# Optimization experiments

Measured on AMD Instinct MI355X. Metric: run time of the kernel, lower is better.

## Reference

```python
import jax, jax.numpy as jnp
import numpy as np

B, S, D, H = 4, 2048, 1024, 16
DK = D // H


def setup_inputs() -> dict:
    key = jax.random.key(0)
    ks = jax.random.split(key, 8)
    q = jax.random.normal(ks[0], (B, S, D), dtype=jnp.float32)
    k = jax.random.normal(ks[1], (B, S, D), dtype=jnp.float32)
    v = jax.random.normal(ks[2], (B, S, D), dtype=jnp.float32)
    mask = jnp.ones((1, 1, S, S), dtype=jnp.int32)
    scale = 1.0 / np.sqrt(D)
    Wq = jax.random.normal(ks[3], (D, D), dtype=jnp.float32) * scale
    Wk = jax.random.normal(ks[4], (D, D), dtype=jnp.float32) * scale
    Wv = jax.random.normal(ks[5], (D, D), dtype=jnp.float32) * scale
    Wo = jax.random.normal(ks[6], (D, D), dtype=jnp.float32) * scale
    return {"q": q, "k": k, "v": v, "mask": mask,
            "Wq": Wq, "Wk": Wk, "Wv": Wv, "Wo": Wo}


def reference(q, k, v, mask, Wq, Wk, Wv, Wo):
    # Linear projections (nn.Linear with bias=False: x @ W.T)
    query = jnp.einsum('bsd,ed->bse', q, Wq).reshape(B, S, H, DK).transpose(0, 2, 1, 3)
    key_ = jnp.einsum('bsd,ed->bse', k, Wk).reshape(B, S, H, DK).transpose(0, 2, 1, 3)
    value = jnp.einsum('bsd,ed->bse', v, Wv).reshape(B, S, H, DK).transpose(0, 2, 1, 3)
    # scores: [B, H, S, S]
    scores = jnp.einsum('bhqd,bhkd->bhqk', query, key_) / jnp.sqrt(jnp.float32(DK))
    scores = jnp.where(mask == 0, jnp.float32(-1e9), scores)
    attn = jax.nn.softmax(scores, axis=-1)
    # context: [B, H, S, DK] -> [B, S, D]
    ctx = jnp.einsum('bhqk,bhkd->bhqd', attn, value)
    ctx = ctx.transpose(0, 2, 1, 3).reshape(B, S, D)
    return jnp.einsum('bsd,ed->bse', ctx, Wo)
```

## Files before the change

### kernel.cpp

```cpp
#include <hip/hip_runtime.h>
#include <hip/hip_bf16.h>
#include <stdint.h>

#define Bb 4
#define Ss 2048
#define Dd 1024
#define Hh 16
#define DK 64

typedef short bf16x8 __attribute__((ext_vector_type(8)));
typedef float f32x4 __attribute__((ext_vector_type(4)));
typedef float f32x16 __attribute__((ext_vector_type(16)));
typedef unsigned short u16;
typedef unsigned int u32;

__device__ __forceinline__ u16 f2bf(float f) {
  u32 u = __float_as_uint(f);
  u32 r = (u + 0x7fffu + ((u >> 16) & 1u)) >> 16;
  return (u16)r;
}

#define CVTPK(d_, lo_, hi_) asm("v_cvt_pk_bf16_f32 %0, %1, %2" : "=v"(d_) : "v"(lo_), "v"(hi_))

#define GLD16(g, l) __builtin_amdgcn_global_load_lds( \
    (const __attribute__((address_space(1))) u32*)(g), \
    (__attribute__((address_space(3))) u32*)(l), 16, 0, 0)

__global__ __launch_bounds__(256) void cvt4_kernel(const float* __restrict__ a, const float* __restrict__ b,
                                                   const float* __restrict__ c, const float* __restrict__ d,
                                                   u16* __restrict__ oa, u16* __restrict__ ob,
                                                   u16* __restrict__ oc, u16* __restrict__ od) {
  int which = blockIdx.y;
  const float* in = which == 0 ? a : which == 1 ? b : which == 2 ? c : d;
  u16* out = which == 0 ? oa : which == 1 ? ob : which == 2 ? oc : od;
  int i = (blockIdx.x * 256 + threadIdx.x) * 4;
  float4 v = *(const float4*)(in + i);
  ushort4 o;
  o.x = f2bf(v.x); o.y = f2bf(v.y); o.z = f2bf(v.z); o.w = f2bf(v.w);
  *(ushort4*)(out + i) = o;
}

__device__ __forceinline__ void regstage_f32(char* dst, const float* __restrict__ src,
                                             int base, int K, int k0, int tid) {
#pragma unroll
  for (int rr = 0; rr < 8; ++rr) {
    int off = rr * 4096 + tid * 16;
    int row = off >> 8;
    int c4 = off & 255;
    f32x4 vv = *(const f32x4*)(src + (size_t)(base + row) * K + k0 + (c4 >> 2));
    u32 lo_, hi_;
    CVTPK(lo_, vv[0], vv[1]);
    CVTPK(hi_, vv[2], vv[3]);
    uint2 val; val.x = lo_; val.y = hi_;
    *(uint2*)(dst + row * 128 + ((c4 >> 1) ^ ((row & 7) << 4))) = val;
  }
}

template <int F32A, int F32W, int OUT_BF16, int TAU, int HEAVY_M>
__device__ __forceinline__ void gemm_body(char* smem, int ord,
                                          const void* __restrict__ Ain,
                                          const void* __restrict__ Win,
                                          void* __restrict__ Cout,
                                          int M, int N, int K, float scale) {
  char* As = smem;
  char* Wl = smem + 16384;
  const int tid = threadIdx.x;
  const int lane = tid & 63;
  const int wv = tid >> 6;
  const int wm = wv >> 1, wn = wv & 1;
  const int heavy = ((ord & 7) << 3) | (ord >> 6);
  const int light = (ord >> 3) & 7;
  const int m0 = (HEAVY_M ? heavy : light) * 128;
  const int n0 = (HEAVY_M ? light : heavy) * 128;

  f32x4 acc[4][4] = {};

  for (int k0 = 0; k0 < K; k0 += 64) {
    if constexpr (F32A) {
      regstage_f32(As, (const float*)Ain, m0, K, k0, tid);
    } else {
      const u16* Ab = (const u16*)Ain;
#pragma unroll
      for (int c = 0; c < 4; ++c) {
        int tb = c * 4096 + tid * 16;
        int row = tb >> 7;
        int sg = (tb & 127) ^ ((row & 7) << 4);
        GLD16(Ab + (size_t)(m0 + row) * K + k0 + (sg >> 1), As + c * 4096 + wv * 1024);
      }
    }
    if constexpr (F32W) {
      regstage_f32(Wl, (const float*)Win, n0, K, k0, tid);
    } else {
      const u16* Wb = (const u16*)Win;
#pragma unroll
      for (int c = 0; c < 4; ++c) {
        int tb = c * 4096 + tid * 16;
        int row = tb >> 7;
        int sg = (tb & 127) ^ ((row & 7) << 4);
        GLD16(Wb + (size_t)(n0 + row) * K + k0 + (sg >> 1), Wl + c * 4096 + wv * 1024);
      }
    }
    __syncthreads();
#pragma unroll
    for (int kk = 0; kk < 2; ++kk) {
      bf16x8 af[4], bfr[4];
#pragma unroll
      for (int mi = 0; mi < 4; ++mi) {
        int r = wm * 64 + mi * 16 + (lane & 15);
        int cb = kk * 64 + (lane >> 4) * 16;
        af[mi] = *(const bf16x8*)(As + r * 128 + (cb ^ ((r & 7) << 4)));
      }
#pragma unroll
      for (int ni = 0; ni < 4; ++ni) {
        int r = wn * 64 + ni * 16 + (lane & 15);
        int cb = kk * 64 + (lane >> 4) * 16;
        bfr[ni] = *(const bf16x8*)(Wl + r * 128 + (cb ^ ((r & 7) << 4)));
      }
#pragma unroll
      for (int mi = 0; mi < 4; ++mi)
#pragma unroll
        for (int ni = 0; ni < 4; ++ni)
          acc[mi][ni] = __builtin_amdgcn_mfma_f32_16x16x32_bf16(af[mi], bfr[ni], acc[mi][ni], 0, 0, 0);
    }
    __syncthreads();
  }
  int l4 = lane & 15;
  int cst = TAU ? ((l4 & 3) | ((l4 & 4) << 1) | ((l4 & 8) >> 1)) : l4;
#pragma unroll
  for (int mi = 0; mi < 4; ++mi) {
#pragma unroll
    for (int i = 0; i < 4; ++i) {
      int row = m0 + wm * 64 + mi * 16 + (lane >> 4) * 4 + i;
#pragma unroll
      for (int ni = 0; ni < 4; ++ni) {
        int col = n0 + wn * 64 + ni * 16 + cst;
        float val = acc[mi][ni][i] * scale;
        if (OUT_BF16)
          ((u16*)Cout)[(size_t)row * N + col] = f2bf(val);
        else
          ((float*)Cout)[(size_t)row * N + col] = val;
      }
    }
  }
}

__global__ __launch_bounds__(256) void proj_fused(const float* __restrict__ q,
                                                  const float* __restrict__ k,
                                                  const float* __restrict__ v,
                                                  const u16* __restrict__ Wqb,
                                                  const u16* __restrict__ Wkb,
                                                  const u16* __restrict__ Wvb,
                                                  u16* __restrict__ Qp,
                                                  u16* __restrict__ Kp,
                                                  u16* __restrict__ VT,
                                                  float qscale) {
  __shared__ __align__(16) char smem[32768];
  const int ord = blockIdx.x;
  const int which = ord >> 9;
  const int local = ord & 511;
  if (which == 0)
    gemm_body<1, 0, 1, 0, 1>(smem, local, q, Wqb, Qp, 8192, 1024, 1024, qscale);
  else if (which == 1)
    gemm_body<1, 0, 1, 0, 1>(smem, local, k, Wkb, Kp, 8192, 1024, 1024, 1.0f);
  else
    gemm_body<0, 1, 1, 1, 0>(smem, local, Wvb, v, VT, 1024, 8192, 1024, 1.0f);
}

__global__ __launch_bounds__(256) void gemm_out(const u16* __restrict__ A,
                                                const u16* __restrict__ W,
                                                float* __restrict__ Cout) {
  __shared__ __align__(16) char smem[32768];
  gemm_body<0, 0, 0, 0, 1>(smem, blockIdx.x, A, W, Cout, 8192, 1024, 1024, 1.0f);
}

#define MAKE_PA(dst, P, R0)                                       \
  {                                                               \
    u32 W0_, W1_, W2_, W3_;                                       \
    CVTPK(W0_, P[R0 + 0], P[R0 + 1]);                             \
    CVTPK(W1_, P[R0 + 2], P[R0 + 3]);                             \
    CVTPK(W2_, P[R0 + 4], P[R0 + 5]);                             \
    CVTPK(W3_, P[R0 + 6], P[R0 + 7]);                             \
    union { u32 w[4]; bf16x8 v; } u_;                             \
    u_.w[0] = W0_; u_.w[1] = W1_; u_.w[2] = W2_; u_.w[3] = W3_;   \
    dst = u_.v;                                                   \
  }

__global__ __launch_bounds__(512) void attn_kernel(const u16* __restrict__ Q,
                                                   const u16* __restrict__ Kp,
                                                   const u16* __restrict__ VT,
                                                   u16* __restrict__ ctx) {
  __shared__ __align__(16) char lds[32768];
  const int tid = threadIdx.x;
  const int lane = tid & 63;
  const int w = tid >> 6;
  const int hi = lane >> 5;
  const int lq = lane & 31;
  const int fid = blockIdx.x;
  const int bh = ((fid >> 6) << 3) | (fid & 7);
  const int qb = (fid >> 3) & 7;
  const int b = bh >> 4;
  const int h = bh & 15;
  const int q0 = qb * 256 + w * 32;

  const u16* qptr = Q + ((size_t)(b * Ss + q0 + lq)) * Dd + h * DK + hi * 8;
  bf16x8 qf[4];
#pragma unroll
  for (int ds = 0; ds < 4; ++ds) qf[ds] = *(const bf16x8*)(qptr + ds * 16);

  const int t16 = tid * 16;
  const int srow = t16 >> 7;
  const int colB = t16 & 127;
  const int scolB = colB ^ ((srow & 7) << 4);
  const u16* ksrc = Kp + ((size_t)(b * Ss + srow)) * Dd + h * DK + (scolB >> 1);
  const u16* vsrc = VT + ((size_t)(h * DK + srow)) * (Bb * Ss) + b * Ss + (scolB >> 1);

  f32x16 o0 = {}, o1 = {};
  float lsum = 0.f;
  const int xk = (lq & 7) << 4;

  GLD16(ksrc, lds + w * 1024);
  GLD16(vsrc, lds + 8192 + w * 1024);
  __syncthreads();

  for (int t = 0; t < Ss / 64; ++t) {
    const int buf = (t & 1) * 16384;
    if (t + 1 < Ss / 64) {
      const int nbuf = 16384 - buf;
      const size_t s0n = (size_t)(t + 1) * 64;
      GLD16(ksrc + s0n * Dd, lds + nbuf + w * 1024);
      GLD16(vsrc + s0n, lds + nbuf + 8192 + w * 1024);
    }
    f32x16 p0 = {}, p1 = {};
    __builtin_amdgcn_s_setprio(1);
#pragma unroll
    for (int ds = 0; ds < 4; ++ds) {
      const int c = (32 * ds + 16 * hi) ^ xk;
      bf16x8 ka = *(const bf16x8*)(lds + buf + lq * 128 + c);
      bf16x8 kb = *(const bf16x8*)(lds + buf + 4096 + lq * 128 + c);
      p0 = __builtin_amdgcn_mfma_f32_32x32x16_bf16(ka, qf[ds], p0, 0, 0, 0);
      p1 = __builtin_amdgcn_mfma_f32_32x32x16_bf16(kb, qf[ds], p1, 0, 0, 0);
    }
    __builtin_amdgcn_s_setprio(0);
    bf16x8 va0 = *(const bf16x8*)(lds + buf + 8192 + lq * 128 + ((16 * hi) ^ xk));
    bf16x8 vb0 = *(const bf16x8*)(lds + buf + 8192 + 4096 + lq * 128 + ((16 * hi) ^ xk));
    float s16[16];
#pragma unroll
    for (int r = 0; r < 16; ++r) {
      p0[r] = __builtin_amdgcn_exp2f(p0[r]);
      p1[r] = __builtin_amdgcn_exp2f(p1[r]);
      s16[r] = p0[r] + p1[r];
    }
#pragma unroll
    for (int r = 0; r < 8; ++r) s16[r] += s16[r + 8];
#pragma unroll
    for (int r = 0; r < 4; ++r) s16[r] += s16[r + 4];
    lsum += (s16[0] + s16[2]) + (s16[1] + s16[3]);
    bf16x8 pa[4];
    MAKE_PA(pa[0], p0, 0);
    MAKE_PA(pa[1], p0, 8);
    MAKE_PA(pa[2], p1, 0);
    MAKE_PA(pa[3], p1, 8);
    __builtin_amdgcn_sched_barrier(0);
    asm volatile("s_nop 3");
    __builtin_amdgcn_s_setprio(1);
    o0 = __builtin_amdgcn_mfma_f32_32x32x16_bf16(va0, pa[0], o0, 0, 0, 0);
    o1 = __builtin_amdgcn_mfma_f32_32x32x16_bf16(vb0, pa[0], o1, 0, 0, 0);
#pragma unroll
    for (int ks = 1; ks < 4; ++ks) {
      const int c = (32 * ks + 16 * hi) ^ xk;
      bf16x8 va = *(const bf16x8*)(lds + buf + 8192 + lq * 128 + c);
      bf16x8 vb = *(const bf16x8*)(lds + buf + 8192 + 4096 + lq * 128 + c);
      o0 = __builtin_amdgcn_mfma_f32_32x32x16_bf16(va, pa[ks], o0, 0, 0, 0);
      o1 = __builtin_amdgcn_mfma_f32_32x32x16_bf16(vb, pa[ks], o1, 0, 0, 0);
    }
    __builtin_amdgcn_s_setprio(0);
    __syncthreads();
  }

  lsum += __shfl_xor(lsum, 32);
  float inv = 1.f / lsum;
  u16* cptr = ctx + ((size_t)(b * Ss + q0 + lq)) * Dd + h * DK + 4 * hi;
#pragma unroll
  for (int g = 0; g < 4; ++g) {
    ushort4 s0v, s1v;
    s0v.x = f2bf(o0[4 * g + 0] * inv);
    s0v.y = f2bf(o0[4 * g + 1] * inv);
    s0v.z = f2bf(o0[4 * g + 2] * inv);
    s0v.w = f2bf(o0[4 * g + 3] * inv);
    *(ushort4*)(cptr + 8 * g) = s0v;
    s1v.x = f2bf(o1[4 * g + 0] * inv);
    s1v.y = f2bf(o1[4 * g + 1] * inv);
    s1v.z = f2bf(o1[4 * g + 2] * inv);
    s1v.w = f2bf(o1[4 * g + 3] * inv);
    *(ushort4*)(cptr + 32 + 8 * g) = s1v;
  }
}

extern "C" void kernel_launch(void* const* d_in, const int* in_sizes, int n_in,
                              void* d_out, int out_size, void* d_ws, size_t ws_size,
                              hipStream_t stream) {
  const float* q = (const float*)d_in[0];
  const float* k = (const float*)d_in[1];
  const float* v = (const float*)d_in[2];
  const float* Wq = (const float*)d_in[4];
  const float* Wk = (const float*)d_in[5];
  const float* Wv = (const float*)d_in[6];
  const float* Wo = (const float*)d_in[7];

  u16* wsp = (u16*)d_ws;
  const size_t DDsz = (size_t)Dd * Dd;
  const size_t BSD = (size_t)Bb * Ss * Dd;
  u16* Wqb = wsp;
  u16* Wkb = wsp + DDsz;
  u16* Wvb = wsp + 2 * DDsz;
  u16* Wob = wsp + 3 * DDsz;
  u16* Qp = wsp + 4 * DDsz;
  u16* Kp = Qp + BSD;
  u16* VT = Kp + BSD;
  u16* Xb = VT + BSD;

  dim3 blk(256);
  cvt4_kernel<<<dim3(DDsz / 1024, 4), blk, 0, stream>>>(Wq, Wk, Wv, Wo, Wqb, Wkb, Wvb, Wob);

  const float QSCALE = 0.125f * 1.4426950408889634f;
  proj_fused<<<dim3(1536), blk, 0, stream>>>(q, k, v, Wqb, Wkb, Wvb, Qp, Kp, VT, QSCALE);

  attn_kernel<<<dim3(512), dim3(512), 0, stream>>>(Qp, Kp, VT, Xb);

  gemm_out<<<dim3(512), blk, 0, stream>>>(Xb, Wob, (float*)d_out);
}
```

Before: 197.5 us.

## Split attention KV loop across two wave halves and merge partial outputs in LDS

The attention block grows to 1024 threads. Each half of the waves handles half of the key/value sequence for the same 256 queries, using its own double-buffered LDS region. Partial outputs and row sums are combined through LDS at the end. This halves the serial KV loop length per wave and raises wave-level parallelism, at the cost of doubled LDS, extra syncs, and duplicated Q loads. There is no running max, so exp values are summed directly, which is valid because the softmax has no max subtraction.

```diff
diff --git a/kernel.cpp b/kernel.cpp
--- a/kernel.cpp
+++ b/kernel.cpp
@@ -185,14 +185,16 @@
     dst = u_.v;                                                   \
   }
 
-__global__ __launch_bounds__(512) void attn_kernel(const u16* __restrict__ Q,
-                                                   const u16* __restrict__ Kp,
-                                                   const u16* __restrict__ VT,
-                                                   u16* __restrict__ ctx) {
-  __shared__ __align__(16) char lds[32768];
+__global__ __launch_bounds__(1024, 8) void attn_kernel(const u16* __restrict__ Q,
+                                                       const u16* __restrict__ Kp,
+                                                       const u16* __restrict__ VT,
+                                                       u16* __restrict__ ctx) {
+  __shared__ __align__(64) char lds[65536];
   const int tid = threadIdx.x;
   const int lane = tid & 63;
   const int w = tid >> 6;
+  const int half = w >> 3;
+  const int qw = w & 7;
   const int hi = lane >> 5;
   const int lq = lane & 31;
   const int fid = blockIdx.x;
@@ -200,36 +202,40 @@
   const int qb = (fid >> 3) & 7;
   const int b = bh >> 4;
   const int h = bh & 15;
-  const int q0 = qb * 256 + w * 32;
+  const int q0 = qb * 256 + qw * 32;
 
   const u16* qptr = Q + ((size_t)(b * Ss + q0 + lq)) * Dd + h * DK + hi * 8;
   bf16x8 qf[4];
 #pragma unroll
   for (int ds = 0; ds < 4; ++ds) qf[ds] = *(const bf16x8*)(qptr + ds * 16);
 
-  const int t16 = tid * 16;
+  const int tl = tid & 511;
+  const int t16 = tl * 16;
   const int srow = t16 >> 7;
   const int colB = t16 & 127;
   const int scolB = colB ^ ((srow & 7) << 4);
   const u16* ksrc = Kp + ((size_t)(b * Ss + srow)) * Dd + h * DK + (scolB >> 1);
   const u16* vsrc = VT + ((size_t)(h * DK + srow)) * (Bb * Ss) + b * Ss + (scolB >> 1);
+  const int hbase = half * 32768;
+  const int wb = (tl >> 6) * 1024;
 
   f32x16 o0 = {}, o1 = {};
   float lsum = 0.f;
   const int xk = (lq & 7) << 4;
-
-  GLD16(ksrc, lds + w * 1024);
-  GLD16(vsrc, lds + 8192 + w * 1024);
+  const int tb0 = half * 16;
+
+#define STAGE_T(T, s) {                                                   \
+    size_t roff = (size_t)(T) * 64;                                       \
+    GLD16(ksrc + roff * Dd, lds + hbase + (s) * 16384 + wb);              \
+    GLD16(vsrc + roff, lds + hbase + (s) * 16384 + 8192 + wb);            \
+  }
+
+  STAGE_T(tb0, 0)
   __syncthreads();
 
-  for (int t = 0; t < Ss / 64; ++t) {
-    const int buf = (t & 1) * 16384;
-    if (t + 1 < Ss / 64) {
-      const int nbuf = 16384 - buf;
-      const size_t s0n = (size_t)(t + 1) * 64;
-      GLD16(ksrc + s0n * Dd, lds + nbuf + w * 1024);
-      GLD16(vsrc + s0n, lds + nbuf + 8192 + w * 1024);
-    }
+  for (int i = 0; i < 16; ++i) {
+    const int buf = hbase + (i & 1) * 16384;
+    if (i < 15) STAGE_T(tb0 + i + 1, (i + 1) & 1)
     f32x16 p0 = {}, p1 = {};
     __builtin_amdgcn_s_setprio(1);
 #pragma unroll
@@ -278,22 +284,43 @@
   }
 
   lsum += __shfl_xor(lsum, 32);
-  float inv = 1.f / lsum;
-  u16* cptr = ctx + ((size_t)(b * Ss + q0 + lq)) * Dd + h * DK + 4 * hi;
-#pragma unroll
-  for (int g = 0; g < 4; ++g) {
-    ushort4 s0v, s1v;
-    s0v.x = f2bf(o0[4 * g + 0] * inv);
-    s0v.y = f2bf(o0[4 * g + 1] * inv);
-    s0v.z = f2bf(o0[4 * g + 2] * inv);
-    s0v.w = f2bf(o0[4 * g + 3] * inv);
-    *(ushort4*)(cptr + 8 * g) = s0v;
-    s1v.x = f2bf(o1[4 * g + 0] * inv);
-    s1v.y = f2bf(o1[4 * g + 1] * inv);
-    s1v.z = f2bf(o1[4 * g + 2] * inv);
-    s1v.w = f2bf(o1[4 * g + 3] * inv);
-    *(ushort4*)(cptr + 32 + 8 * g) = s1v;
-  }
+
+  f32x16* ex = (f32x16*)lds;
+  float* exl = (float*)(lds + 32768);
+  if (half) {
+    ex[(w - 8) * 64 + lane] = o0;
+    exl[(w - 8) * 64 + lane] = lsum;
+  }
+  __syncthreads();
+  f32x16 oB0 = {};
+  float lB = 0.f;
+  if (!half) {
+    oB0 = ex[w * 64 + lane];
+    lB = exl[w * 64 + lane];
+  }
+  __syncthreads();
+  if (half) ex[(w - 8) * 64 + lane] = o1;
+  __syncthreads();
+  if (!half) {
+    f32x16 oB1 = ex[w * 64 + lane];
+    float inv = 1.f / (lsum + lB);
+    u16* cptr = ctx + ((size_t)(b * Ss + q0 + lq)) * Dd + h * DK + 4 * hi;
+#pragma unroll
+    for (int g = 0; g < 4; ++g) {
+      ushort4 s0v, s1v;
+      s0v.x = f2bf((o0[4 * g + 0] + oB0[4 * g + 0]) * inv);
+      s0v.y = f2bf((o0[4 * g + 1] + oB0[4 * g + 1]) * inv);
+      s0v.z = f2bf((o0[4 * g + 2] + oB0[4 * g + 2]) * inv);
+      s0v.w = f2bf((o0[4 * g + 3] + oB0[4 * g + 3]) * inv);
+      *(ushort4*)(cptr + 8 * g) = s0v;
+      s1v.x = f2bf((o1[4 * g + 0] + oB1[4 * g + 0]) * inv);
+      s1v.y = f2bf((o1[4 * g + 1] + oB1[4 * g + 1]) * inv);
+      s1v.z = f2bf((o1[4 * g + 2] + oB1[4 * g + 2]) * inv);
+      s1v.w = f2bf((o1[4 * g + 3] + oB1[4 * g + 3]) * inv);
+      *(ushort4*)(cptr + 32 + 8 * g) = s1v;
+    }
+  }
+#undef STAGE_T
 }
 
 extern "C" void kernel_launch(void* const* d_in, const int* in_sizes, int n_in,
@@ -325,7 +352,7 @@
   const float QSCALE = 0.125f * 1.4426950408889634f;
   proj_fused<<<dim3(1536), blk, 0, stream>>>(q, k, v, Wqb, Wkb, Wvb, Qp, Kp, VT, QSCALE);
 
-  attn_kernel<<<dim3(512), dim3(512), 0, stream>>>(Qp, Kp, VT, Xb);
+  attn_kernel<<<dim3(512), dim3(1024), 0, stream>>>(Qp, Kp, VT, Xb);
 
   gemm_out<<<dim3(512), blk, 0, stream>>>(Xb, Wob, (float*)d_out);
 }
```

Result: slower. 563.2 us (+185.1%).

## Process two KV tiles per barrier with four-slot LDS ring in attention

Applied to the files above, without the earlier changes.

The attention loop now stages two 64-row K/V tiles per iteration into a four-slot LDS ring (64KB) and computes both tiles between barriers. This halves the number of __syncthreads per head and issues prefetches two tiles ahead, aiming to hide global load latency and barrier stalls. The cost is doubled LDS use per block, which may reduce occupancy, and more code from the unrolled macro bodies.

```diff
diff --git a/kernel.cpp b/kernel.cpp
--- a/kernel.cpp
+++ b/kernel.cpp
@@ -185,11 +185,13 @@
     dst = u_.v;                                                   \
   }
 
+#define SLOT(U) (((((U) >> 1) & 1) << 15) | (((U) & 1) << 14))
+
 __global__ __launch_bounds__(512) void attn_kernel(const u16* __restrict__ Q,
                                                    const u16* __restrict__ Kp,
                                                    const u16* __restrict__ VT,
                                                    u16* __restrict__ ctx) {
-  __shared__ __align__(16) char lds[32768];
+  __shared__ __align__(16) char lds[65536];
   const int tid = threadIdx.x;
   const int lane = tid & 63;
   const int w = tid >> 6;
@@ -217,63 +219,73 @@
   f32x16 o0 = {}, o1 = {};
   float lsum = 0.f;
   const int xk = (lq & 7) << 4;
-
-  GLD16(ksrc, lds + w * 1024);
-  GLD16(vsrc, lds + 8192 + w * 1024);
+  const int wb = w * 1024;
+
+#define STAGE_U(U) {                                               \
+    size_t ro = (size_t)(U) * 64;                                  \
+    GLD16(ksrc + ro * Dd, lds + SLOT(U) + wb);                     \
+    GLD16(vsrc + ro, lds + SLOT(U) + 8192 + wb);                   \
+  }
+
+#define ATTN_TILE(BASE) {                                                             \
+    const int buf_ = (BASE);                                                          \
+    f32x16 p0 = {}, p1 = {};                                                          \
+    __builtin_amdgcn_s_setprio(1);                                                    \
+    _Pragma("unroll")                                                                 \
+    for (int ds = 0; ds < 4; ++ds) {                                                  \
+      const int c = (32 * ds + 16 * hi) ^ xk;                                         \
+      bf16x8 ka = *(const bf16x8*)(lds + buf_ + lq * 128 + c);                        \
+      bf16x8 kb = *(const bf16x8*)(lds + buf_ + 4096 + lq * 128 + c);                 \
+      p0 = __builtin_amdgcn_mfma_f32_32x32x16_bf16(ka, qf[ds], p0, 0, 0, 0);          \
+      p1 = __builtin_amdgcn_mfma_f32_32x32x16_bf16(kb, qf[ds], p1, 0, 0, 0);          \
+    }                                                                                 \
+    __builtin_amdgcn_s_setprio(0);                                                    \
+    bf16x8 va0 = *(const bf16x8*)(lds + buf_ + 8192 + lq * 128 + ((16 * hi) ^ xk));   \
+    bf16x8 vb0 = *(const bf16x8*)(lds + buf_ + 8192 + 4096 + lq * 128 + ((16 * hi) ^ xk)); \
+    float s16[16];                                                                    \
+    _Pragma("unroll")                                                                 \
+    for (int r = 0; r < 16; ++r) {                                                    \
+      p0[r] = __builtin_amdgcn_exp2f(p0[r]);                                          \
+      p1[r] = __builtin_amdgcn_exp2f(p1[r]);                                          \
+      s16[r] = p0[r] + p1[r];                                                         \
+    }                                                                                 \
+    _Pragma("unroll")                                                                 \
+    for (int r = 0; r < 8; ++r) s16[r] += s16[r + 8];                                 \
+    _Pragma("unroll")                                                                 \
+    for (int r = 0; r < 4; ++r) s16[r] += s16[r + 4];                                 \
+    lsum += (s16[0] + s16[2]) + (s16[1] + s16[3]);                                    \
+    bf16x8 pa[4];                                                                     \
+    MAKE_PA(pa[0], p0, 0);                                                            \
+    MAKE_PA(pa[1], p0, 8);                                                            \
+    MAKE_PA(pa[2], p1, 0);                                                            \
+    MAKE_PA(pa[3], p1, 8);                                                            \
+    __builtin_amdgcn_sched_barrier(0);                                                \
+    asm volatile("s_nop 3");                                                          \
+    __builtin_amdgcn_s_setprio(1);                                                    \
+    o0 = __builtin_amdgcn_mfma_f32_32x32x16_bf16(va0, pa[0], o0, 0, 0, 0);            \
+    o1 = __builtin_amdgcn_mfma_f32_32x32x16_bf16(vb0, pa[0], o1, 0, 0, 0);            \
+    _Pragma("unroll")                                                                 \
+    for (int ks = 1; ks < 4; ++ks) {                                                  \
+      const int c = (32 * ks + 16 * hi) ^ xk;                                         \
+      bf16x8 va = *(const bf16x8*)(lds + buf_ + 8192 + lq * 128 + c);                 \
+      bf16x8 vb = *(const bf16x8*)(lds + buf_ + 8192 + 4096 + lq * 128 + c);          \
+      o0 = __builtin_amdgcn_mfma_f32_32x32x16_bf16(va, pa[ks], o0, 0, 0, 0);          \
+      o1 = __builtin_amdgcn_mfma_f32_32x32x16_bf16(vb, pa[ks], o1, 0, 0, 0);          \
+    }                                                                                 \
+    __builtin_amdgcn_s_setprio(0);                                                    \
+  }
+
+  STAGE_U(0)
+  STAGE_U(1)
   __syncthreads();
 
-  for (int t = 0; t < Ss / 64; ++t) {
-    const int buf = (t & 1) * 16384;
-    if (t + 1 < Ss / 64) {
-      const int nbuf = 16384 - buf;
-      const size_t s0n = (size_t)(t + 1) * 64;
-      GLD16(ksrc + s0n * Dd, lds + nbuf + w * 1024);
-      GLD16(vsrc + s0n, lds + nbuf + 8192 + w * 1024);
-    }
-    f32x16 p0 = {}, p1 = {};
-    __builtin_amdgcn_s_setprio(1);
-#pragma unroll
-    for (int ds = 0; ds < 4; ++ds) {
-      const int c = (32 * ds + 16 * hi) ^ xk;
-      bf16x8 ka = *(const bf16x8*)(lds + buf + lq * 128 + c);
-      bf16x8 kb = *(const bf16x8*)(lds + buf + 4096 + lq * 128 + c);
-      p0 = __builtin_amdgcn_mfma_f32_32x32x16_bf16(ka, qf[ds], p0, 0, 0, 0);
-      p1 = __builtin_amdgcn_mfma_f32_32x32x16_bf16(kb, qf[ds], p1, 0, 0, 0);
-    }
-    __builtin_amdgcn_s_setprio(0);
-    bf16x8 va0 = *(const bf16x8*)(lds + buf + 8192 + lq * 128 + ((16 * hi) ^ xk));
-    bf16x8 vb0 = *(const bf16x8*)(lds + buf + 8192 + 4096 + lq * 128 + ((16 * hi) ^ xk));
-    float s16[16];
-#pragma unroll
-    for (int r = 0; r < 16; ++r) {
-      p0[r] = __builtin_amdgcn_exp2f(p0[r]);
-      p1[r] = __builtin_amdgcn_exp2f(p1[r]);
-      s16[r] = p0[r] + p1[r];
-    }
-#pragma unroll
-    for (int r = 0; r < 8; ++r) s16[r] += s16[r + 8];
-#pragma unroll
-    for (int r = 0; r < 4; ++r) s16[r] += s16[r + 4];
-    lsum += (s16[0] + s16[2]) + (s16[1] + s16[3]);
-    bf16x8 pa[4];
-    MAKE_PA(pa[0], p0, 0);
-    MAKE_PA(pa[1], p0, 8);
-    MAKE_PA(pa[2], p1, 0);
-    MAKE_PA(pa[3], p1, 8);
-    __builtin_amdgcn_sched_barrier(0);
-    asm volatile("s_nop 3");
-    __builtin_amdgcn_s_setprio(1);
-    o0 = __builtin_amdgcn_mfma_f32_32x32x16_bf16(va0, pa[0], o0, 0, 0, 0);
-    o1 = __builtin_amdgcn_mfma_f32_32x32x16_bf16(vb0, pa[0], o1, 0, 0, 0);
-#pragma unroll
-    for (int ks = 1; ks < 4; ++ks) {
-      const int c = (32 * ks + 16 * hi) ^ xk;
-      bf16x8 va = *(const bf16x8*)(lds + buf + 8192 + lq * 128 + c);
-      bf16x8 vb = *(const bf16x8*)(lds + buf + 8192 + 4096 + lq * 128 + c);
-      o0 = __builtin_amdgcn_mfma_f32_32x32x16_bf16(va, pa[ks], o0, 0, 0, 0);
-      o1 = __builtin_amdgcn_mfma_f32_32x32x16_bf16(vb, pa[ks], o1, 0, 0, 0);
-    }
-    __builtin_amdgcn_s_setprio(0);
+  for (int t = 0; t < 16; ++t) {
+    if (t < 15) {
+      STAGE_U(2 * t + 2)
+      STAGE_U(2 * t + 3)
+    }
+    ATTN_TILE(SLOT(2 * t))
+    ATTN_TILE(SLOT(2 * t + 1))
     __syncthreads();
   }
 
@@ -294,6 +306,8 @@
     s1v.w = f2bf(o1[4 * g + 3] * inv);
     *(ushort4*)(cptr + 32 + 8 * g) = s1v;
   }
+#undef STAGE_U
+#undef ATTN_TILE
 }
 
 extern "C" void kernel_launch(void* const* d_in, const int* in_sizes, int n_in,
```

New measurement: 195.5 us. No clear change (-1.0%).
